# Performance work log

Hardware: AMD Instinct MI355X
Metric: run time of the kernel (lower is better)

Reference implementation:

```python
import jax, jax.numpy as jnp
import numpy as np

N_NODES = 50000
N_EDGES = 800000
D = 64


def setup_inputs() -> dict:
    key = jax.random.key(0)
    ks = jax.random.split(key, 8)
    x = jax.random.normal(ks[0], (N_NODES, D), dtype=jnp.float32)
    edge_index = jax.random.randint(ks[1], (2, N_EDGES), 0, N_NODES, dtype=jnp.int64)
    # GCNConv params (PyG: Linear without bias inside lin, bias added after aggregation)
    def glorot(k, fan_in, fan_out):
        lim = (6.0 / (fan_in + fan_out)) ** 0.5
        return jax.random.uniform(k, (fan_in, fan_out), jnp.float32, -lim, lim)
    W1 = glorot(ks[2], D, D); b1 = jnp.zeros((D,), jnp.float32)
    W2 = glorot(ks[3], D, D); b2 = jnp.zeros((D,), jnp.float32)
    W3 = glorot(ks[4], D, D); b3 = jnp.zeros((D,), jnp.float32)
    return {"x": x, "edge_index": edge_index,
            "W1": W1, "b1": b1, "W2": W2, "b2": b2, "W3": W3, "b3": b3}


def _gcn_norm(edge_index, n_nodes, dtype):
    # Add self-loops, compute symmetric normalization D^-1/2 (A+I) D^-1/2 (PyG GCNConv default).
    loop = jnp.arange(n_nodes, dtype=edge_index.dtype)
    src = jnp.concatenate([edge_index[0], loop])  # message source j
    dst = jnp.concatenate([edge_index[1], loop])  # aggregation target i
    deg = jax.ops.segment_sum(jnp.ones_like(dst, dtype=dtype), dst, num_segments=n_nodes)
    dinv = jnp.where(deg > 0, jax.lax.rsqrt(deg), 0.0)
    norm = dinv[src] * dinv[dst]  # [E + N]
    return src, dst, norm


def _gcn_conv(x, src, dst, norm, W, b, n_nodes):
    h = x @ W                              # [N, D_out]
    msg = h[src] * norm[:, None]           # gather + scale, [E+N, D_out]
    out = jax.ops.segment_sum(msg, dst, num_segments=n_nodes)  # scatter-add
    return out + b


def reference(x, edge_index, W1, b1, W2, b2, W3, b3):
    n = x.shape[0]
    src, dst, norm = _gcn_norm(edge_index, n, x.dtype)
    # layer 0: conv -> relu -> residual
    h = _gcn_conv(x, src, dst, norm, W1, b1, n)
    h = jax.nn.relu(h) + x
    # layer 1: conv -> relu -> residual
    r = h
    h = _gcn_conv(h, src, dst, norm, W2, b2, n)
    h = jax.nn.relu(h) + r
    # layer 2 (final): conv only
    h = _gcn_conv(h, src, dst, norm, W3, b3, n)
    return h
```

## Files before the change

### kernel.cpp

```cpp
#include <hip/hip_runtime.h>
#include <hip/hip_bf16.h>


#define CAP 64
#define EDGE_CHUNK 1024

typedef __attribute__((ext_vector_type(8))) short bf16x8;
typedef __attribute__((ext_vector_type(4))) float f32x4;

__device__ inline unsigned pack_bf16(float a, float b) {
    union { float f; unsigned i; } ua, ub;
    ua.f = a; ub.f = b;
    unsigned x = (ua.i + 0x7fffu + ((ua.i >> 16) & 1u)) >> 16;
    unsigned y = (ub.i + 0x7fffu + ((ub.i >> 16) & 1u)) >> 16;
    return x | (y << 16);
}
__device__ inline unsigned short to_bf16(float a) {
    union { float f; unsigned i; } u; u.f = a;
    return (unsigned short)((u.i + 0x7fffu + ((u.i >> 16) & 1u)) >> 16);
}
__device__ inline void acc_bf16x2(unsigned u, float& a, float& b) {
    union { unsigned i; float f; } lo, hi;
    lo.i = u << 16;
    hi.i = u & 0xffff0000u;
    a += lo.f; b += hi.f;
}

__global__ void fill_kernel(const int* __restrict__ src, const int* __restrict__ dst,
                            int* __restrict__ cnt, int* __restrict__ adj,
                            int E, int npc) {
    int cls = blockIdx.x & 7;
    int base = (blockIdx.x >> 3) * EDGE_CHUNK;
    int end = min(base + EDGE_CHUNK, E);
    int lo = cls * npc, hi = lo + npc;
    for (int e = base + threadIdx.x; e < end; e += blockDim.x) {
        int d = dst[e];
        if (d >= lo && d < hi) {
            int p = atomicAdd(&cnt[d], 1);
            adj[(size_t)d * CAP + p] = src[e];
        }
    }
}

__device__ inline void stage_W(const float* __restrict__ W, unsigned short* Wb, int t) {
#pragma unroll
    for (int e0 = 0; e0 < 2; e0++) {
        int e = t + e0 * 256;
        int sc = e >> 6;
        int l  = e & 63;
        int s = sc >> 2, c = sc & 3;
        int nn = c * 16 + (l & 15);
        int kb = s * 32 + (l >> 4) * 8;
        const float* wp = &W[(size_t)kb * 64 + nn];
        unsigned q0 = pack_bf16(wp[0 * 64], wp[1 * 64]);
        unsigned q1 = pack_bf16(wp[2 * 64], wp[3 * 64]);
        unsigned q2 = pack_bf16(wp[4 * 64], wp[5 * 64]);
        unsigned q3 = pack_bf16(wp[6 * 64], wp[7 * 64]);
        *(uint4*)&Wb[e * 8] = make_uint4(q0, q1, q2, q3);
    }
}

__global__ __launch_bounds__(256) void gemm_kernel(const float* __restrict__ in,
                                                   const float* __restrict__ W,
                                                   const int* __restrict__ cnt,
                                                   unsigned short* __restrict__ g, int n) {
    __shared__ unsigned short Wb[512 * 8];
    int t = threadIdx.x;
    stage_W(W, Wb, t);

    int wv = t >> 6;
    int lane = t & 63;
    int quad = lane >> 4;
    int m16 = lane & 15;

    int rowA = blockIdx.x * 64 + wv * 16 + m16;
    union { bf16x8 v; uint4 u; } a0, a1;
    {
        float4 f0 = make_float4(0, 0, 0, 0), f1 = f0, f2 = f0, f3 = f0;
        if (rowA < n) {
            const float* rp = &in[(size_t)rowA * 64];
            f0 = *(const float4*)&rp[quad * 8];
            f1 = *(const float4*)&rp[quad * 8 + 4];
            f2 = *(const float4*)&rp[32 + quad * 8];
            f3 = *(const float4*)&rp[32 + quad * 8 + 4];
        }
        a0.u = make_uint4(pack_bf16(f0.x, f0.y), pack_bf16(f0.z, f0.w),
                          pack_bf16(f1.x, f1.y), pack_bf16(f1.z, f1.w));
        a1.u = make_uint4(pack_bf16(f2.x, f2.y), pack_bf16(f2.z, f2.w),
                          pack_bf16(f3.x, f3.y), pack_bf16(f3.z, f3.w));
    }
    __syncthreads();

    f32x4 acc[4];
#pragma unroll
    for (int c = 0; c < 4; c++) {
        bf16x8 b0 = *(const bf16x8*)&Wb[((size_t)(0 * 4 + c) * 64 + lane) * 8];
        bf16x8 b1 = *(const bf16x8*)&Wb[((size_t)(1 * 4 + c) * 64 + lane) * 8];
        f32x4 z = {0.f, 0.f, 0.f, 0.f};
        z = __builtin_amdgcn_mfma_f32_16x16x32_bf16(a0.v, b0, z, 0, 0, 0);
        z = __builtin_amdgcn_mfma_f32_16x16x32_bf16(a1.v, b1, z, 0, 0, 0);
        acc[c] = z;
    }

    int rowbase = blockIdx.x * 64 + wv * 16 + quad * 4;
    float dv[4];
#pragma unroll
    for (int r = 0; r < 4; r++) {
        int row = rowbase + r;
        dv[r] = (row < n) ? rsqrtf((float)(cnt[row] + 1)) : 0.f;
    }
#pragma unroll
    for (int c = 0; c < 4; c++) {
#pragma unroll
        for (int r = 0; r < 4; r++) {
            int row = rowbase + r;
            if (row < n)
                g[(size_t)row * 64 + c * 16 + m16] = to_bf16(acc[c][r] * dv[r]);
        }
    }
}

template <int WRITE_H>
__global__ __launch_bounds__(256) void aggemm_kernel(
        const unsigned short* __restrict__ g_in,
        const int* __restrict__ cnt,
        const int* __restrict__ adj,
        const float* __restrict__ bias,
        const float* __restrict__ res,
        const float* __restrict__ W,
        float* __restrict__ h_out,
        unsigned short* __restrict__ g_out,
        int n) {
    __shared__ unsigned short Wb[512 * 8];
    __shared__ unsigned short Afrag[512 * 8];
    int t = threadIdx.x;
    stage_W(W, Wb, t);

    int np = t >> 4;
    int lg = t & 15;
    const int c4 = lg * 4;
    int chunk = lg >> 1;
    int half  = lg & 1;
#pragma unroll 1
    for (int p = 0; p < 4; p++) {
        int i = blockIdx.x * 64 + p * 16 + np;
        float vx = 0.f, vy = 0.f, vz = 0.f, vw = 0.f;
        if (i < n) {
            int deg = cnt[i];
            const int* lst = adj + (size_t)i * CAP;
            float4 rr = *(const float4*)&res[(size_t)i * 64 + c4];
            float ax = 0.f, ay = 0.f, az = 0.f, aw = 0.f;
            {
                uint2 v = *(const uint2*)&g_in[(size_t)i * 64 + c4];
                acc_bf16x2(v.x, ax, ay);
                acc_bf16x2(v.y, az, aw);
            }
            int k = 0;
            for (; k + 8 <= deg; k += 8) {
                int4 ja = *(const int4*)&lst[k];
                int4 jb = *(const int4*)&lst[k + 4];
                uint2 v0 = *(const uint2*)&g_in[(size_t)ja.x * 64 + c4];
                uint2 v1 = *(const uint2*)&g_in[(size_t)ja.y * 64 + c4];
                uint2 v2 = *(const uint2*)&g_in[(size_t)ja.z * 64 + c4];
                uint2 v3 = *(const uint2*)&g_in[(size_t)ja.w * 64 + c4];
                uint2 v4 = *(const uint2*)&g_in[(size_t)jb.x * 64 + c4];
                uint2 v5 = *(const uint2*)&g_in[(size_t)jb.y * 64 + c4];
                uint2 v6 = *(const uint2*)&g_in[(size_t)jb.z * 64 + c4];
                uint2 v7 = *(const uint2*)&g_in[(size_t)jb.w * 64 + c4];
                acc_bf16x2(v0.x, ax, ay); acc_bf16x2(v0.y, az, aw);
                acc_bf16x2(v1.x, ax, ay); acc_bf16x2(v1.y, az, aw);
                acc_bf16x2(v2.x, ax, ay); acc_bf16x2(v2.y, az, aw);
                acc_bf16x2(v3.x, ax, ay); acc_bf16x2(v3.y, az, aw);
                acc_bf16x2(v4.x, ax, ay); acc_bf16x2(v4.y, az, aw);
                acc_bf16x2(v5.x, ax, ay); acc_bf16x2(v5.y, az, aw);
                acc_bf16x2(v6.x, ax, ay); acc_bf16x2(v6.y, az, aw);
                acc_bf16x2(v7.x, ax, ay); acc_bf16x2(v7.y, az, aw);
            }
            if (k + 4 <= deg) {
                int4 ja = *(const int4*)&lst[k];
                uint2 v0 = *(const uint2*)&g_in[(size_t)ja.x * 64 + c4];
                uint2 v1 = *(const uint2*)&g_in[(size_t)ja.y * 64 + c4];
                uint2 v2 = *(const uint2*)&g_in[(size_t)ja.z * 64 + c4];
                uint2 v3 = *(const uint2*)&g_in[(size_t)ja.w * 64 + c4];
                acc_bf16x2(v0.x, ax, ay); acc_bf16x2(v0.y, az, aw);
                acc_bf16x2(v1.x, ax, ay); acc_bf16x2(v1.y, az, aw);
                acc_bf16x2(v2.x, ax, ay); acc_bf16x2(v2.y, az, aw);
                acc_bf16x2(v3.x, ax, ay); acc_bf16x2(v3.y, az, aw);
                k += 4;
            }
            for (; k < deg; k++) {
                uint2 v = *(const uint2*)&g_in[(size_t)lst[k] * 64 + c4];
                acc_bf16x2(v.x, ax, ay);
                acc_bf16x2(v.y, az, aw);
            }
            float dvv = rsqrtf((float)(deg + 1));
            float4 bb = *(const float4*)&bias[c4];
            vx = fmaxf(dvv * ax + bb.x, 0.f) + rr.x;
            vy = fmaxf(dvv * ay + bb.y, 0.f) + rr.y;
            vz = fmaxf(dvv * az + bb.z, 0.f) + rr.z;
            vw = fmaxf(dvv * aw + bb.w, 0.f) + rr.w;
            if (WRITE_H) {
                float4 hv = make_float4(vx, vy, vz, vw);
                *(float4*)&h_out[(size_t)i * 64 + c4] = hv;
            }
        }
        uint2 pk;
        pk.x = pack_bf16(vx, vy);
        pk.y = pack_bf16(vz, vw);
        *(uint2*)&Afrag[(((size_t)(p * 8 + chunk) * 16 + np) * 8) + half * 4] = pk;
    }
    __syncthreads();

    int wv = t >> 6;
    int lane = t & 63;
    int quad = lane >> 4;
    int m16 = lane & 15;
    bf16x8 a0 = *(const bf16x8*)&Afrag[((size_t)(wv * 8 + quad) * 16 + m16) * 8];
    bf16x8 a1 = *(const bf16x8*)&Afrag[((size_t)(wv * 8 + 4 + quad) * 16 + m16) * 8];
    f32x4 acc[4];
#pragma unroll
    for (int c = 0; c < 4; c++) {
        bf16x8 b0 = *(const bf16x8*)&Wb[((size_t)(0 * 4 + c) * 64 + lane) * 8];
        bf16x8 b1 = *(const bf16x8*)&Wb[((size_t)(1 * 4 + c) * 64 + lane) * 8];
        f32x4 z = {0.f, 0.f, 0.f, 0.f};
        z = __builtin_amdgcn_mfma_f32_16x16x32_bf16(a0, b0, z, 0, 0, 0);
        z = __builtin_amdgcn_mfma_f32_16x16x32_bf16(a1, b1, z, 0, 0, 0);
        acc[c] = z;
    }
    int rowbase = blockIdx.x * 64 + wv * 16 + quad * 4;
    float dv2[4];
#pragma unroll
    for (int r = 0; r < 4; r++) {
        int row = rowbase + r;
        dv2[r] = (row < n) ? rsqrtf((float)(cnt[row] + 1)) : 0.f;
    }
#pragma unroll
    for (int c = 0; c < 4; c++) {
#pragma unroll
        for (int r = 0; r < 4; r++) {
            int row = rowbase + r;
            if (row < n)
                g_out[(size_t)row * 64 + c * 16 + m16] = to_bf16(acc[c][r] * dv2[r]);
        }
    }
}

__global__ __launch_bounds__(256) void agg_kernel(const unsigned short* __restrict__ g,
                                                  const int* __restrict__ cnt,
                                                  const int* __restrict__ adj,
                                                  const float* __restrict__ bias,
                                                  float* __restrict__ out, int n) {
    int t = threadIdx.x;
    int lg = t & 7;
    int i = blockIdx.x * 32 + (t >> 3);
    if (i >= n) return;
    int deg = cnt[i];
    const int* lst = adj + (size_t)i * CAP;
    const int c8 = lg * 8;
    size_t rowoff = (size_t)i * 64 + c8;
    float a0 = 0.f, a1 = 0.f, a2 = 0.f, a3 = 0.f;
    float a4 = 0.f, a5 = 0.f, a6 = 0.f, a7 = 0.f;
    {
        uint4 v = *(const uint4*)&g[(size_t)i * 64 + c8];
        acc_bf16x2(v.x, a0, a1); acc_bf16x2(v.y, a2, a3);
        acc_bf16x2(v.z, a4, a5); acc_bf16x2(v.w, a6, a7);
    }
    int k = 0;
    for (; k + 8 <= deg; k += 8) {
        int4 ja = *(const int4*)&lst[k];
        int4 jb = *(const int4*)&lst[k + 4];
        uint4 v0 = *(const uint4*)&g[(size_t)ja.x * 64 + c8];
        uint4 v1 = *(const uint4*)&g[(size_t)ja.y * 64 + c8];
        uint4 v2 = *(const uint4*)&g[(size_t)ja.z * 64 + c8];
        uint4 v3 = *(const uint4*)&g[(size_t)ja.w * 64 + c8];
        uint4 v4 = *(const uint4*)&g[(size_t)jb.x * 64 + c8];
        uint4 v5 = *(const uint4*)&g[(size_t)jb.y * 64 + c8];
        uint4 v6 = *(const uint4*)&g[(size_t)jb.z * 64 + c8];
        uint4 v7 = *(const uint4*)&g[(size_t)jb.w * 64 + c8];
        acc_bf16x2(v0.x, a0, a1); acc_bf16x2(v0.y, a2, a3);
        acc_bf16x2(v0.z, a4, a5); acc_bf16x2(v0.w, a6, a7);
        acc_bf16x2(v1.x, a0, a1); acc_bf16x2(v1.y, a2, a3);
        acc_bf16x2(v1.z, a4, a5); acc_bf16x2(v1.w, a6, a7);
        acc_bf16x2(v2.x, a0, a1); acc_bf16x2(v2.y, a2, a3);
        acc_bf16x2(v2.z, a4, a5); acc_bf16x2(v2.w, a6, a7);
        acc_bf16x2(v3.x, a0, a1); acc_bf16x2(v3.y, a2, a3);
        acc_bf16x2(v3.z, a4, a5); acc_bf16x2(v3.w, a6, a7);
        acc_bf16x2(v4.x, a0, a1); acc_bf16x2(v4.y, a2, a3);
        acc_bf16x2(v4.z, a4, a5); acc_bf16x2(v4.w, a6, a7);
        acc_bf16x2(v5.x, a0, a1); acc_bf16x2(v5.y, a2, a3);
        acc_bf16x2(v5.z, a4, a5); acc_bf16x2(v5.w, a6, a7);
        acc_bf16x2(v6.x, a0, a1); acc_bf16x2(v6.y, a2, a3);
        acc_bf16x2(v6.z, a4, a5); acc_bf16x2(v6.w, a6, a7);
        acc_bf16x2(v7.x, a0, a1); acc_bf16x2(v7.y, a2, a3);
        acc_bf16x2(v7.z, a4, a5); acc_bf16x2(v7.w, a6, a7);
    }
    if (k + 4 <= deg) {
        int4 ja = *(const int4*)&lst[k];
        uint4 v0 = *(const uint4*)&g[(size_t)ja.x * 64 + c8];
        uint4 v1 = *(const uint4*)&g[(size_t)ja.y * 64 + c8];
        uint4 v2 = *(const uint4*)&g[(size_t)ja.z * 64 + c8];
        uint4 v3 = *(const uint4*)&g[(size_t)ja.w * 64 + c8];
        acc_bf16x2(v0.x, a0, a1); acc_bf16x2(v0.y, a2, a3);
        acc_bf16x2(v0.z, a4, a5); acc_bf16x2(v0.w, a6, a7);
        acc_bf16x2(v1.x, a0, a1); acc_bf16x2(v1.y, a2, a3);
        acc_bf16x2(v1.z, a4, a5); acc_bf16x2(v1.w, a6, a7);
        acc_bf16x2(v2.x, a0, a1); acc_bf16x2(v2.y, a2, a3);
        acc_bf16x2(v2.z, a4, a5); acc_bf16x2(v2.w, a6, a7);
        acc_bf16x2(v3.x, a0, a1); acc_bf16x2(v3.y, a2, a3);
        acc_bf16x2(v3.z, a4, a5); acc_bf16x2(v3.w, a6, a7);
        k += 4;
    }
    for (; k < deg; k++) {
        uint4 v = *(const uint4*)&g[(size_t)lst[k] * 64 + c8];
        acc_bf16x2(v.x, a0, a1); acc_bf16x2(v.y, a2, a3);
        acc_bf16x2(v.z, a4, a5); acc_bf16x2(v.w, a6, a7);
    }
    float dv = rsqrtf((float)(deg + 1));
    float4 b0 = *(const float4*)&bias[c8];
    float4 b1 = *(const float4*)&bias[c8 + 4];
    float4 o0, o1;
    o0.x = dv * a0 + b0.x; o0.y = dv * a1 + b0.y;
    o0.z = dv * a2 + b0.z; o0.w = dv * a3 + b0.w;
    o1.x = dv * a4 + b1.x; o1.y = dv * a5 + b1.y;
    o1.z = dv * a6 + b1.z; o1.w = dv * a7 + b1.w;
    *(float4*)&out[rowoff] = o0;
    *(float4*)&out[rowoff + 4] = o1;
}

extern "C" void kernel_launch(void* const* d_in, const int* in_sizes, int n_in,
                              void* d_out, int out_size, void* d_ws, size_t ws_size,
                              hipStream_t stream) {
    const float* x  = (const float*)d_in[0];
    const int*   ei = (const int*)d_in[1];
    const float* W1 = (const float*)d_in[2];
    const float* b1 = (const float*)d_in[3];
    const float* W2 = (const float*)d_in[4];
    const float* b2 = (const float*)d_in[5];
    const float* W3 = (const float*)d_in[6];
    const float* b3 = (const float*)d_in[7];
    float* out = (float*)d_out;

    const int N = in_sizes[0] / 64;
    const int E = in_sizes[1] / 2;
    const int* src = ei;
    const int* dst = ei + E;
    const int npc = (N + 7) / 8;
    const int nEdgeChunks = (E + EDGE_CHUNK - 1) / EDGE_CHUNK;

    char* p = (char*)d_ws;
    int*            cnt = (int*)p;            p += ((N + 63) / 64) * 64 * 4;
    int*            adj = (int*)p;            p += ((size_t)N + 1) * CAP * 4;
    unsigned short* ga  = (unsigned short*)p; p += (size_t)N * 64 * 2;
    unsigned short* gb  = (unsigned short*)p; p += (size_t)N * 64 * 2;
    float*          h1  = (float*)p;          p += (size_t)N * 64 * 4;

    const int tileBlocks = (N + 63) / 64;
    const int aggBlocks  = (N + 31) / 32;

    hipMemsetAsync(cnt, 0, (size_t)N * 4, stream);
    fill_kernel<<<nEdgeChunks * 8, 256, 0, stream>>>(src, dst, cnt, adj, E, npc);

    gemm_kernel<<<tileBlocks, 256, 0, stream>>>(x, W1, cnt, ga, N);
    aggemm_kernel<1><<<tileBlocks, 256, 0, stream>>>(ga, cnt, adj, b1, x, W2, h1, gb, N);
    aggemm_kernel<0><<<tileBlocks, 256, 0, stream>>>(gb, cnt, adj, b2, h1, W3, nullptr, ga, N);
    agg_kernel<<<aggBlocks, 256, 0, stream>>>(ga, cnt, adj, b3, out, N);
}
```

Measured before the change: 195.9 us.

## Process 32 nodes per aggemm block with 8 lanes and 16-byte gathers

```diff
diff --git a/kernel.cpp b/kernel.cpp
--- a/kernel.cpp
+++ b/kernel.cpp
@@ -121,7 +121,7 @@
 }
 
 template <int WRITE_H>
-__global__ __launch_bounds__(256) void aggemm_kernel(
+__global__ __launch_bounds__(256, 4) void aggemm_kernel(
         const unsigned short* __restrict__ g_in,
         const int* __restrict__ cnt,
         const int* __restrict__ adj,
@@ -132,82 +132,102 @@
         unsigned short* __restrict__ g_out,
         int n) {
     __shared__ unsigned short Wb[512 * 8];
-    __shared__ unsigned short Afrag[512 * 8];
+    __shared__ unsigned short Afrag[256 * 8];
     int t = threadIdx.x;
     stage_W(W, Wb, t);
 
-    int np = t >> 4;
-    int lg = t & 15;
-    const int c4 = lg * 4;
-    int chunk = lg >> 1;
-    int half  = lg & 1;
-#pragma unroll 1
-    for (int p = 0; p < 4; p++) {
-        int i = blockIdx.x * 64 + p * 16 + np;
-        float vx = 0.f, vy = 0.f, vz = 0.f, vw = 0.f;
-        if (i < n) {
-            int deg = cnt[i];
-            const int* lst = adj + (size_t)i * CAP;
-            float4 rr = *(const float4*)&res[(size_t)i * 64 + c4];
-            float ax = 0.f, ay = 0.f, az = 0.f, aw = 0.f;
-            {
-                uint2 v = *(const uint2*)&g_in[(size_t)i * 64 + c4];
-                acc_bf16x2(v.x, ax, ay);
-                acc_bf16x2(v.y, az, aw);
-            }
-            int k = 0;
-            for (; k + 8 <= deg; k += 8) {
-                int4 ja = *(const int4*)&lst[k];
-                int4 jb = *(const int4*)&lst[k + 4];
-                uint2 v0 = *(const uint2*)&g_in[(size_t)ja.x * 64 + c4];
-                uint2 v1 = *(const uint2*)&g_in[(size_t)ja.y * 64 + c4];
-                uint2 v2 = *(const uint2*)&g_in[(size_t)ja.z * 64 + c4];
-                uint2 v3 = *(const uint2*)&g_in[(size_t)ja.w * 64 + c4];
-                uint2 v4 = *(const uint2*)&g_in[(size_t)jb.x * 64 + c4];
-                uint2 v5 = *(const uint2*)&g_in[(size_t)jb.y * 64 + c4];
-                uint2 v6 = *(const uint2*)&g_in[(size_t)jb.z * 64 + c4];
-                uint2 v7 = *(const uint2*)&g_in[(size_t)jb.w * 64 + c4];
-                acc_bf16x2(v0.x, ax, ay); acc_bf16x2(v0.y, az, aw);
-                acc_bf16x2(v1.x, ax, ay); acc_bf16x2(v1.y, az, aw);
-                acc_bf16x2(v2.x, ax, ay); acc_bf16x2(v2.y, az, aw);
-                acc_bf16x2(v3.x, ax, ay); acc_bf16x2(v3.y, az, aw);
-                acc_bf16x2(v4.x, ax, ay); acc_bf16x2(v4.y, az, aw);
-                acc_bf16x2(v5.x, ax, ay); acc_bf16x2(v5.y, az, aw);
-                acc_bf16x2(v6.x, ax, ay); acc_bf16x2(v6.y, az, aw);
-                acc_bf16x2(v7.x, ax, ay); acc_bf16x2(v7.y, az, aw);
-            }
-            if (k + 4 <= deg) {
-                int4 ja = *(const int4*)&lst[k];
-                uint2 v0 = *(const uint2*)&g_in[(size_t)ja.x * 64 + c4];
-                uint2 v1 = *(const uint2*)&g_in[(size_t)ja.y * 64 + c4];
-                uint2 v2 = *(const uint2*)&g_in[(size_t)ja.z * 64 + c4];
-                uint2 v3 = *(const uint2*)&g_in[(size_t)ja.w * 64 + c4];
-                acc_bf16x2(v0.x, ax, ay); acc_bf16x2(v0.y, az, aw);
-                acc_bf16x2(v1.x, ax, ay); acc_bf16x2(v1.y, az, aw);
-                acc_bf16x2(v2.x, ax, ay); acc_bf16x2(v2.y, az, aw);
-                acc_bf16x2(v3.x, ax, ay); acc_bf16x2(v3.y, az, aw);
-                k += 4;
-            }
-            for (; k < deg; k++) {
-                uint2 v = *(const uint2*)&g_in[(size_t)lst[k] * 64 + c4];
-                acc_bf16x2(v.x, ax, ay);
-                acc_bf16x2(v.y, az, aw);
-            }
-            float dvv = rsqrtf((float)(deg + 1));
-            float4 bb = *(const float4*)&bias[c4];
-            vx = fmaxf(dvv * ax + bb.x, 0.f) + rr.x;
-            vy = fmaxf(dvv * ay + bb.y, 0.f) + rr.y;
-            vz = fmaxf(dvv * az + bb.z, 0.f) + rr.z;
-            vw = fmaxf(dvv * aw + bb.w, 0.f) + rr.w;
-            if (WRITE_H) {
-                float4 hv = make_float4(vx, vy, vz, vw);
-                *(float4*)&h_out[(size_t)i * 64 + c4] = hv;
-            }
-        }
-        uint2 pk;
-        pk.x = pack_bf16(vx, vy);
-        pk.y = pack_bf16(vz, vw);
-        *(uint2*)&Afrag[(((size_t)(p * 8 + chunk) * 16 + np) * 8) + half * 4] = pk;
+    int r  = t >> 3;
+    int lg = t & 7;
+    const int c8 = lg * 8;
+    int i = blockIdx.x * 32 + r;
+    float v0 = 0.f, v1 = 0.f, v2 = 0.f, v3 = 0.f;
+    float v4 = 0.f, v5 = 0.f, v6 = 0.f, v7 = 0.f;
+    if (i < n) {
+        int deg = cnt[i];
+        const int* lst = adj + (size_t)i * CAP;
+        float4 rr0 = *(const float4*)&res[(size_t)i * 64 + c8];
+        float4 rr1 = *(const float4*)&res[(size_t)i * 64 + c8 + 4];
+        float a0 = 0.f, a1 = 0.f, a2 = 0.f, a3 = 0.f;
+        float a4 = 0.f, a5 = 0.f, a6 = 0.f, a7 = 0.f;
+        {
+            uint4 v = *(const uint4*)&g_in[(size_t)i * 64 + c8];
+            acc_bf16x2(v.x, a0, a1); acc_bf16x2(v.y, a2, a3);
+            acc_bf16x2(v.z, a4, a5); acc_bf16x2(v.w, a6, a7);
+        }
+        int k = 0;
+        for (; k + 8 <= deg; k += 8) {
+            int4 ja = *(const int4*)&lst[k];
+            int4 jb = *(const int4*)&lst[k + 4];
+            uint4 w0 = *(const uint4*)&g_in[(size_t)ja.x * 64 + c8];
+            uint4 w1 = *(const uint4*)&g_in[(size_t)ja.y * 64 + c8];
+            uint4 w2 = *(const uint4*)&g_in[(size_t)ja.z * 64 + c8];
+            uint4 w3 = *(const uint4*)&g_in[(size_t)ja.w * 64 + c8];
+            uint4 w4 = *(const uint4*)&g_in[(size_t)jb.x * 64 + c8];
+            uint4 w5 = *(const uint4*)&g_in[(size_t)jb.y * 64 + c8];
+            uint4 w6 = *(const uint4*)&g_in[(size_t)jb.z * 64 + c8];
+            uint4 w7 = *(const uint4*)&g_in[(size_t)jb.w * 64 + c8];
+            acc_bf16x2(w0.x, a0, a1); acc_bf16x2(w0.y, a2, a3);
+            acc_bf16x2(w0.z, a4, a5); acc_bf16x2(w0.w, a6, a7);
+            acc_bf16x2(w1.x, a0, a1); acc_bf16x2(w1.y, a2, a3);
+            acc_bf16x2(w1.z, a4, a5); acc_bf16x2(w1.w, a6, a7);
+            acc_bf16x2(w2.x, a0, a1); acc_bf16x2(w2.y, a2, a3);
+            acc_bf16x2(w2.z, a4, a5); acc_bf16x2(w2.w, a6, a7);
+            acc_bf16x2(w3.x, a0, a1); acc_bf16x2(w3.y, a2, a3);
+            acc_bf16x2(w3.z, a4, a5); acc_bf16x2(w3.w, a6, a7);
+            acc_bf16x2(w4.x, a0, a1); acc_bf16x2(w4.y, a2, a3);
+            acc_bf16x2(w4.z, a4, a5); acc_bf16x2(w4.w, a6, a7);
+            acc_bf16x2(w5.x, a0, a1); acc_bf16x2(w5.y, a2, a3);
+            acc_bf16x2(w5.z, a4, a5); acc_bf16x2(w5.w, a6, a7);
+            acc_bf16x2(w6.x, a0, a1); acc_bf16x2(w6.y, a2, a3);
+            acc_bf16x2(w6.z, a4, a5); acc_bf16x2(w6.w, a6, a7);
+            acc_bf16x2(w7.x, a0, a1); acc_bf16x2(w7.y, a2, a3);
+            acc_bf16x2(w7.z, a4, a5); acc_bf16x2(w7.w, a6, a7);
+        }
+        if (k + 4 <= deg) {
+            int4 ja = *(const int4*)&lst[k];
+            uint4 w0 = *(const uint4*)&g_in[(size_t)ja.x * 64 + c8];
+            uint4 w1 = *(const uint4*)&g_in[(size_t)ja.y * 64 + c8];
+            uint4 w2 = *(const uint4*)&g_in[(size_t)ja.z * 64 + c8];
+            uint4 w3 = *(const uint4*)&g_in[(size_t)ja.w * 64 + c8];
+            acc_bf16x2(w0.x, a0, a1); acc_bf16x2(w0.y, a2, a3);
+            acc_bf16x2(w0.z, a4, a5); acc_bf16x2(w0.w, a6, a7);
+            acc_bf16x2(w1.x, a0, a1); acc_bf16x2(w1.y, a2, a3);
+            acc_bf16x2(w1.z, a4, a5); acc_bf16x2(w1.w, a6, a7);
+            acc_bf16x2(w2.x, a0, a1); acc_bf16x2(w2.y, a2, a3);
+            acc_bf16x2(w2.z, a4, a5); acc_bf16x2(w2.w, a6, a7);
+            acc_bf16x2(w3.x, a0, a1); acc_bf16x2(w3.y, a2, a3);
+            acc_bf16x2(w3.z, a4, a5); acc_bf16x2(w3.w, a6, a7);
+            k += 4;
+        }
+        for (; k < deg; k++) {
+            uint4 v = *(const uint4*)&g_in[(size_t)lst[k] * 64 + c8];
+            acc_bf16x2(v.x, a0, a1); acc_bf16x2(v.y, a2, a3);
+            acc_bf16x2(v.z, a4, a5); acc_bf16x2(v.w, a6, a7);
+        }
+        float dvv = rsqrtf((float)(deg + 1));
+        float4 b0 = *(const float4*)&bias[c8];
+        float4 b1 = *(const float4*)&bias[c8 + 4];
+        v0 = fmaxf(dvv * a0 + b0.x, 0.f) + rr0.x;
+        v1 = fmaxf(dvv * a1 + b0.y, 0.f) + rr0.y;
+        v2 = fmaxf(dvv * a2 + b0.z, 0.f) + rr0.z;
+        v3 = fmaxf(dvv * a3 + b0.w, 0.f) + rr0.w;
+        v4 = fmaxf(dvv * a4 + b1.x, 0.f) + rr1.x;
+        v5 = fmaxf(dvv * a5 + b1.y, 0.f) + rr1.y;
+        v6 = fmaxf(dvv * a6 + b1.z, 0.f) + rr1.z;
+        v7 = fmaxf(dvv * a7 + b1.w, 0.f) + rr1.w;
+        if (WRITE_H) {
+            *(float4*)&h_out[(size_t)i * 64 + c8]     = make_float4(v0, v1, v2, v3);
+            *(float4*)&h_out[(size_t)i * 64 + c8 + 4] = make_float4(v4, v5, v6, v7);
+        }
+    }
+    {
+        uint4 pk;
+        pk.x = pack_bf16(v0, v1);
+        pk.y = pack_bf16(v2, v3);
+        pk.z = pack_bf16(v4, v5);
+        pk.w = pack_bf16(v6, v7);
+        int sA = r >> 4, mA = r & 15;
+        *(uint4*)&Afrag[((size_t)(sA * 8 + lg) * 16 + mA) * 8] = pk;
     }
     __syncthreads();
 
@@ -215,32 +235,36 @@
     int lane = t & 63;
     int quad = lane >> 4;
     int m16 = lane & 15;
-    bf16x8 a0 = *(const bf16x8*)&Afrag[((size_t)(wv * 8 + quad) * 16 + m16) * 8];
-    bf16x8 a1 = *(const bf16x8*)&Afrag[((size_t)(wv * 8 + 4 + quad) * 16 + m16) * 8];
-    f32x4 acc[4];
-#pragma unroll
-    for (int c = 0; c < 4; c++) {
+    int sB = wv & 1;
+    int ch = wv >> 1;
+    bf16x8 af0 = *(const bf16x8*)&Afrag[((size_t)(sB * 8 + quad) * 16 + m16) * 8];
+    bf16x8 af1 = *(const bf16x8*)&Afrag[((size_t)(sB * 8 + 4 + quad) * 16 + m16) * 8];
+    f32x4 acc[2];
+#pragma unroll
+    for (int c2 = 0; c2 < 2; c2++) {
+        int c = ch * 2 + c2;
         bf16x8 b0 = *(const bf16x8*)&Wb[((size_t)(0 * 4 + c) * 64 + lane) * 8];
         bf16x8 b1 = *(const bf16x8*)&Wb[((size_t)(1 * 4 + c) * 64 + lane) * 8];
         f32x4 z = {0.f, 0.f, 0.f, 0.f};
-        z = __builtin_amdgcn_mfma_f32_16x16x32_bf16(a0, b0, z, 0, 0, 0);
-        z = __builtin_amdgcn_mfma_f32_16x16x32_bf16(a1, b1, z, 0, 0, 0);
-        acc[c] = z;
-    }
-    int rowbase = blockIdx.x * 64 + wv * 16 + quad * 4;
+        z = __builtin_amdgcn_mfma_f32_16x16x32_bf16(af0, b0, z, 0, 0, 0);
+        z = __builtin_amdgcn_mfma_f32_16x16x32_bf16(af1, b1, z, 0, 0, 0);
+        acc[c2] = z;
+    }
+    int rowbase = blockIdx.x * 32 + sB * 16 + quad * 4;
     float dv2[4];
 #pragma unroll
-    for (int r = 0; r < 4; r++) {
-        int row = rowbase + r;
-        dv2[r] = (row < n) ? rsqrtf((float)(cnt[row] + 1)) : 0.f;
-    }
-#pragma unroll
-    for (int c = 0; c < 4; c++) {
-#pragma unroll
-        for (int r = 0; r < 4; r++) {
-            int row = rowbase + r;
+    for (int rr = 0; rr < 4; rr++) {
+        int row = rowbase + rr;
+        dv2[rr] = (row < n) ? rsqrtf((float)(cnt[row] + 1)) : 0.f;
+    }
+#pragma unroll
+    for (int c2 = 0; c2 < 2; c2++) {
+        int c = ch * 2 + c2;
+#pragma unroll
+        for (int rr = 0; rr < 4; rr++) {
+            int row = rowbase + rr;
             if (row < n)
-                g_out[(size_t)row * 64 + c * 16 + m16] = to_bf16(acc[c][r] * dv2[r]);
+                g_out[(size_t)row * 64 + c * 16 + m16] = to_bf16(acc[c2][rr] * dv2[rr]);
         }
     }
 }
@@ -355,13 +379,13 @@
     float*          h1  = (float*)p;          p += (size_t)N * 64 * 4;
 
     const int tileBlocks = (N + 63) / 64;
-    const int aggBlocks  = (N + 31) / 32;
+    const int halfBlocks = (N + 31) / 32;
 
     hipMemsetAsync(cnt, 0, (size_t)N * 4, stream);
     fill_kernel<<<nEdgeChunks * 8, 256, 0, stream>>>(src, dst, cnt, adj, E, npc);
 
     gemm_kernel<<<tileBlocks, 256, 0, stream>>>(x, W1, cnt, ga, N);
-    aggemm_kernel<1><<<tileBlocks, 256, 0, stream>>>(ga, cnt, adj, b1, x, W2, h1, gb, N);
-    aggemm_kernel<0><<<tileBlocks, 256, 0, stream>>>(gb, cnt, adj, b2, h1, W3, nullptr, ga, N);
-    agg_kernel<<<aggBlocks, 256, 0, stream>>>(ga, cnt, adj, b3, out, N);
-}
+    aggemm_kernel<1><<<halfBlocks, 256, 0, stream>>>(ga, cnt, adj, b1, x, W2, h1, gb, N);
+    aggemm_kernel<0><<<halfBlocks, 256, 0, stream>>>(gb, cnt, adj, b2, h1, W3, nullptr, ga, N);
+    agg_kernel<<<halfBlocks, 256, 0, stream>>>(ga, cnt, adj, b3, out, N);
+}
```

After: 187.4 us. -4.4%, faster.
